# Optimization experiments

Measured on AMD Instinct MI355X. Metric: run time of the kernel, lower is better.

The kernel has to match this reference:

```python
import jax, jax.numpy as jnp
import numpy as np

APERTURE = 128
LN_EPS = 1e-6

def _layer_norm(y, g, b):
    mu = jnp.mean(y, axis=-1, keepdims=True)
    var = jnp.var(y, axis=-1, keepdims=True)
    return (y - mu) / jnp.sqrt(var + LN_EPS) * g + b

def setup_inputs() -> dict:
    key = jax.random.key(0)
    ks = jax.random.split(key, 12)
    B, S, D = 4, 4096, 1024
    gain = np.sqrt(2.0)
    xav = lambda k, fan_out, fan_in: jax.random.uniform(
        k, (fan_out, fan_in), jnp.float32,
        -gain * np.sqrt(6.0 / (fan_in + fan_out)), gain * np.sqrt(6.0 / (fan_in + fan_out)))
    return {
        "x": jax.random.normal(ks[0], (B, S, D), jnp.float32),
        "Wq": xav(ks[1], D, D),
        "Wk": xav(ks[2], D, D),
        "Wv": xav(ks[3], D, D),
        "Wo": xav(ks[4], D, D),
        "k1_w": xav(ks[5], D, D),
        "k1_b": jnp.full((D,), 0.1, jnp.float32),
        "k2_w": xav(ks[6], 1, D),
        "k2_b": jnp.full((1,), 0.1, jnp.float32),
        "ln_g": jnp.ones((D,), jnp.float32),
        "ln_b": jnp.zeros((D,), jnp.float32),
    }

def reference(x, Wq, Wk, Wv, Wo, k1_w, k1_b, k2_w, k2_b, ln_g, ln_b):
    B, S, D = x.shape
    scale = jnp.float32(1.0 / np.sqrt(D))
    neg_inf = jnp.float32(-np.inf)

    Q = x @ Wq.T  # [B,S,D]
    K = x @ Wk.T
    V = x @ Wv.T

    e = jnp.einsum('bsd,btd->bst', Q, K) * scale  # [B,S,S]

    # ignore_self: -inf on the diagonal
    i = jnp.arange(S)[:, None]
    j = jnp.arange(S)[None, :]
    e = jnp.where(i == j, neg_inf, e)

    # banded aperture mask: tril(e, ap) * triu(e, -ap); zeros of the product -> -inf
    d = j - i
    scope = jnp.where(d <= APERTURE, e, 0.0) * jnp.where(d >= -APERTURE, e, 0.0)
    e = jnp.where(scope == 0.0, neg_inf, e)

    alpha = jax.nn.softmax(e, axis=2)
    c = jnp.einsum('bst,btd->bsd', alpha, V)
    c = c @ Wo.T

    y = c + x
    y = _layer_norm(y, ln_g, ln_b)
    y = jax.nn.relu(y @ k1_w.T + k1_b)
    y = _layer_norm(y, ln_g, ln_b)
    y = jax.nn.sigmoid(y @ k2_w.T + k2_b)  # [B,S,1]
    return y.reshape(B, S)
```

## Files before the change

### kernel.cpp

```cpp
#include <hip/hip_runtime.h>
#include <math.h>

#define DD 1024
#define SS 4096
#define AP 128
#define LN_EPS 1e-6f
#define BK 32
#define BAND 384

typedef __bf16 bf16;
typedef __attribute__((ext_vector_type(4))) __bf16 bf16x4;
typedef __attribute__((ext_vector_type(8))) __bf16 bf16x8;
typedef __attribute__((ext_vector_type(4))) float f32x4;

#define GLOAD_LDS16(g, l)                                                   \
    __builtin_amdgcn_global_load_lds(                                        \
        (const __attribute__((address_space(1))) void*)(g),                  \
        (__attribute__((address_space(3))) void*)(l), 16, 0, 0)

__global__ __launch_bounds__(256) void cast_f2b(const float* __restrict__ s,
                                                bf16* __restrict__ d) {
    const int i = (blockIdx.x * 256 + threadIdx.x) * 4;
    const float4 a = *(const float4*)(s + i);
    bf16x4 o;
    o[0] = (__bf16)a.x; o[1] = (__bf16)a.y; o[2] = (__bf16)a.z; o[3] = (__bf16)a.w;
    *(bf16x4*)(d + i) = o;
}

__global__ __launch_bounds__(256) void prep_w(const float* __restrict__ Wo,
                                              const float* __restrict__ k1w,
                                              const float* __restrict__ lng,
                                              const float* __restrict__ Wq,
                                              const float* __restrict__ Wk,
                                              const float* __restrict__ Wv,
                                              bf16* __restrict__ Wob,
                                              bf16* __restrict__ k1g,
                                              bf16* __restrict__ Wtb) {
    const int z = blockIdx.y;
    if (z < 2) {
        const float* s = z ? k1w : Wo;
        bf16* d = z ? k1g : Wob;
        const int i = (blockIdx.x * 256 + threadIdx.x) * 4;
        float4 a = *(const float4*)(s + i);
        if (z) {
            const float4 g4 = *(const float4*)(lng + (i & (DD - 1)));
            a.x *= g4.x; a.y *= g4.y; a.z *= g4.z; a.w *= g4.w;
        }
        bf16x4 o;
        o[0] = (__bf16)a.x; o[1] = (__bf16)a.y; o[2] = (__bf16)a.z; o[3] = (__bf16)a.w;
        *(bf16x4*)(d + i) = o;
        return;
    }
    if (blockIdx.x >= 256) return;
    __shared__ float tile[64][65];
    const float* in = (z == 2) ? Wq : (z == 3) ? Wk : Wv;
    bf16* out = Wtb + ((size_t)(z - 2) << 20);
    const int r0 = (blockIdx.x >> 4) * 64, c0 = (blockIdx.x & 15) * 64;
    const int lr = threadIdx.x >> 4;
    const int lc = (threadIdx.x & 15) * 4;
#pragma unroll
    for (int rr = 0; rr < 4; rr++) {
        const int row = lr + rr * 16;
        const float4 v = *(const float4*)(in + (size_t)(r0 + row) * DD + c0 + lc);
        tile[row][lc] = v.x; tile[row][lc + 1] = v.y;
        tile[row][lc + 2] = v.z; tile[row][lc + 3] = v.w;
    }
    __syncthreads();
#pragma unroll
    for (int rr = 0; rr < 4; rr++) {
        const int row = lr + rr * 16;
        bf16x4 o;
        o[0] = (__bf16)tile[lc + 0][row];
        o[1] = (__bf16)tile[lc + 1][row];
        o[2] = (__bf16)tile[lc + 2][row];
        o[3] = (__bf16)tile[lc + 3][row];
        *(bf16x4*)(out + (size_t)(c0 + row) * DD + r0 + lc) = o;
    }
}

__global__ __launch_bounds__(256) void prep_vec(const float* __restrict__ k1w,
                                                const float* __restrict__ lng,
                                                const float* __restrict__ lnb,
                                                const float* __restrict__ k1b,
                                                float* __restrict__ u1,
                                                float* __restrict__ c1b) {
    const int lane = threadIdx.x & 63, wave = threadIdx.x >> 6;
    const int n = blockIdx.x * 4 + wave;
    const float* row = k1w + (size_t)n * DD + lane * 16;
    float su = 0.f, sb = 0.f;
#pragma unroll
    for (int q = 0; q < 4; q++) {
        const float4 a = *(const float4*)(row + q * 4);
        const float4 g4 = *(const float4*)(lng + lane * 16 + q * 4);
        const float4 b4 = *(const float4*)(lnb + lane * 16 + q * 4);
        su += a.x * g4.x + a.y * g4.y + a.z * g4.z + a.w * g4.w;
        sb += a.x * b4.x + a.y * b4.y + a.z * b4.z + a.w * b4.w;
    }
#pragma unroll
    for (int off = 32; off > 0; off >>= 1) {
        su += __shfl_xor(su, off);
        sb += __shfl_xor(sb, off);
    }
    if (lane == 0) {
        u1[n] = su;
        c1b[n] = sb + k1b[n];
    }
}

__global__ __launch_bounds__(256) void gemm_pair(const bf16* __restrict__ A0,
                                                 const bf16* __restrict__ W0,
                                                 bf16* __restrict__ O0,
                                                 const bf16* __restrict__ A1,
                                                 const bf16* __restrict__ W1,
                                                 bf16* __restrict__ O1) {
    const bf16* A = blockIdx.z ? A1 : A0;
    const bf16* W = blockIdx.z ? W1 : W0;
    bf16* O = blockIdx.z ? O1 : O0;
    __shared__ bf16 As[128 * BK];
    __shared__ bf16 Bs[128 * BK];
    const int tid = threadIdx.x;
    const int lane = tid & 63;
    const int wave = tid >> 6;
    const int wm = wave & 1;
    const int wn = wave >> 1;
    const int m0 = blockIdx.y * 128;
    const int n0 = blockIdx.x * 128;

    const int c = wave * 64 + lane;
    const int ar = c >> 2;
    const int ac = (c & 3) << 3;
    char* AsB = (char*)As;
    char* BsB = (char*)Bs;
    const int lr = lane & 15;
    const int lk = (lane >> 4) << 3;

    f32x4 acc[4][4] = {};

    for (int kt = 0; kt < DD; kt += BK) {
        const bf16* ga0 = A + (size_t)(m0 + ar) * DD + kt + ac;
        const bf16* gb0 = W + (size_t)(n0 + ar) * DD + kt + ac;
        GLOAD_LDS16(ga0, AsB + wave * 1024);
        GLOAD_LDS16(ga0 + (size_t)64 * DD, AsB + 4096 + wave * 1024);
        GLOAD_LDS16(gb0, BsB + wave * 1024);
        GLOAD_LDS16(gb0 + (size_t)64 * DD, BsB + 4096 + wave * 1024);
        __syncthreads();

        bf16x8 af[4], bfr[4];
#pragma unroll
        for (int i = 0; i < 4; i++)
            af[i] = *(const bf16x8*)&As[(wm * 64 + i * 16 + lr) * BK + lk];
#pragma unroll
        for (int j = 0; j < 4; j++)
            bfr[j] = *(const bf16x8*)&Bs[(wn * 64 + j * 16 + lr) * BK + lk];
#pragma unroll
        for (int i = 0; i < 4; i++)
#pragma unroll
            for (int j = 0; j < 4; j++)
                acc[i][j] = __builtin_amdgcn_mfma_f32_16x16x32_bf16(af[i], bfr[j], acc[i][j], 0, 0, 0);
        __syncthreads();
    }

#pragma unroll
    for (int i = 0; i < 4; i++) {
        const int row = m0 + wm * 64 + i * 16 + ((lane >> 4) << 2);
#pragma unroll
        for (int j = 0; j < 4; j++) {
            const int col = n0 + wn * 64 + j * 16 + (lane & 15);
#pragma unroll
            for (int rr = 0; rr < 4; rr++)
                O[(size_t)(row + rr) * DD + col] = (__bf16)acc[i][j][rr];
        }
    }
}

__global__ __launch_bounds__(512) void gemm_uv(const bf16* __restrict__ xb,
                                               const bf16* __restrict__ Gt,
                                               const bf16* __restrict__ W2,
                                               bf16* __restrict__ Ub,
                                               bf16* __restrict__ Vt2) {
    __shared__ bf16 As[256 * BK];
    __shared__ bf16 Bs[128 * BK];
    int id = blockIdx.x;
    const bf16* A;
    const bf16* W;
    bf16* O;
    int m0, n0, ldo;
    if (id < 512) {
        A = xb; W = Gt; O = Ub;
        m0 = (id & 63) * 256; n0 = (id >> 6) * 128; ldo = DD;
    } else {
        id -= 512;
        A = W2; W = xb; O = Vt2;
        m0 = (id >> 7) * 256; n0 = (id & 127) * 128; ldo = 4 * SS;
    }
    const int tid = threadIdx.x;
    const int lane = tid & 63;
    const int wave = tid >> 6;
    const int wm = wave & 3;
    const int wn = wave >> 2;

    const int ar = tid >> 2;
    const int ac = (tid & 3) << 3;
    char* AsB = (char*)As;
    char* BsB = (char*)Bs;
    const int lr = lane & 15;
    const int lk = (lane >> 4) << 3;

    f32x4 acc[4][4] = {};

    for (int kt = 0; kt < DD; kt += BK) {
        const bf16* ga0 = A + (size_t)(m0 + ar) * DD + kt + ac;
        const bf16* gb0 = W + (size_t)(n0 + ar) * DD + kt + ac;
        GLOAD_LDS16(ga0, AsB + wave * 1024);
        GLOAD_LDS16(ga0 + (size_t)128 * DD, AsB + 8192 + wave * 1024);
        GLOAD_LDS16(gb0, BsB + wave * 1024);
        __syncthreads();

        bf16x8 af[4], bfr[4];
#pragma unroll
        for (int i = 0; i < 4; i++)
            af[i] = *(const bf16x8*)&As[(wm * 64 + i * 16 + lr) * BK + lk];
#pragma unroll
        for (int j = 0; j < 4; j++)
            bfr[j] = *(const bf16x8*)&Bs[(wn * 64 + j * 16 + lr) * BK + lk];
#pragma unroll
        for (int i = 0; i < 4; i++)
#pragma unroll
            for (int j = 0; j < 4; j++)
                acc[i][j] = __builtin_amdgcn_mfma_f32_16x16x32_bf16(af[i], bfr[j], acc[i][j], 0, 0, 0);
        __syncthreads();
    }

#pragma unroll
    for (int i = 0; i < 4; i++) {
        const int row = m0 + wm * 64 + i * 16 + ((lane >> 4) << 2);
#pragma unroll
        for (int j = 0; j < 4; j++) {
            const int col = n0 + wn * 64 + j * 16 + (lane & 15);
#pragma unroll
            for (int rr = 0; rr < 4; rr++)
                O[(size_t)(row + rr) * ldo + col] = (__bf16)acc[i][j][rr];
        }
    }
}

__global__ __launch_bounds__(512) void gemm_k1(const bf16* __restrict__ T,
                                               const bf16* __restrict__ k1g,
                                               const float* __restrict__ mu,
                                               const float* __restrict__ rstd,
                                               const float* __restrict__ u1,
                                               const float* __restrict__ c1b,
                                               bf16* __restrict__ H0) {
    __shared__ bf16 As[256 * BK];
    __shared__ bf16 Bs[128 * BK];
    const int m0 = blockIdx.x * 256;
    const int n0 = blockIdx.y * 128;
    const int tid = threadIdx.x;
    const int lane = tid & 63;
    const int wave = tid >> 6;
    const int wm = wave & 3;
    const int wn = wave >> 2;

    const int ar = tid >> 2;
    const int ac = (tid & 3) << 3;
    char* AsB = (char*)As;
    char* BsB = (char*)Bs;
    const int lr = lane & 15;
    const int lk = (lane >> 4) << 3;

    f32x4 acc[4][4] = {};

    for (int kt = 0; kt < DD; kt += BK) {
        const bf16* ga0 = T + (size_t)(m0 + ar) * DD + kt + ac;
        const bf16* gb0 = k1g + (size_t)(n0 + ar) * DD + kt + ac;
        GLOAD_LDS16(ga0, AsB + wave * 1024);
        GLOAD_LDS16(ga0 + (size_t)128 * DD, AsB + 8192 + wave * 1024);
        GLOAD_LDS16(gb0, BsB + wave * 1024);
        __syncthreads();

        bf16x8 af[4], bfr[4];
#pragma unroll
        for (int i = 0; i < 4; i++)
            af[i] = *(const bf16x8*)&As[(wm * 64 + i * 16 + lr) * BK + lk];
#pragma unroll
        for (int j = 0; j < 4; j++)
            bfr[j] = *(const bf16x8*)&Bs[(wn * 64 + j * 16 + lr) * BK + lk];
#pragma unroll
        for (int i = 0; i < 4; i++)
#pragma unroll
            for (int j = 0; j < 4; j++)
                acc[i][j] = __builtin_amdgcn_mfma_f32_16x16x32_bf16(af[i], bfr[j], acc[i][j], 0, 0, 0);
        __syncthreads();
    }

#pragma unroll
    for (int i = 0; i < 4; i++) {
        const int row = m0 + wm * 64 + i * 16 + ((lane >> 4) << 2);
#pragma unroll
        for (int j = 0; j < 4; j++) {
            const int col = n0 + wn * 64 + j * 16 + (lane & 15);
            const float u1c = u1[col];
            const float cbc = c1b[col];
#pragma unroll
            for (int rr = 0; rr < 4; rr++) {
                const int r = row + rr;
                const float v = rstd[r] * (acc[i][j][rr] - mu[r] * u1c) + cbc;
                H0[(size_t)r * DD + col] = (__bf16)fmaxf(v, 0.f);
            }
        }
    }
}

__global__ __launch_bounds__(256) void attn_s_mfma(const bf16* __restrict__ U,
                                                   const bf16* __restrict__ X,
                                                   float* __restrict__ S) {
    __shared__ bf16 As[128 * BK];
    __shared__ bf16 Bs[128 * BK];
    const int tid = threadIdx.x;
    const int lane = tid & 63;
    const int wave = tid >> 6;
    const int wm = wave & 1;
    const int wn = wave >> 1;
    const int t = blockIdx.y;
    const int m0 = t * 128;
    const long w0 = (long)t * 128 - 128 + (long)blockIdx.x * 128;

    const int c = wave * 64 + lane;
    const int ar = c >> 2;
    const int ac = (c & 3) << 3;
    char* AsB = (char*)As;
    char* BsB = (char*)Bs;
    const int lr = lane & 15;
    const int lk = (lane >> 4) << 3;

    f32x4 acc[4][4] = {};

    for (int kt = 0; kt < DD; kt += BK) {
        const bf16* ga0 = U + (size_t)(m0 + ar) * DD + kt + ac;
        const bf16* gb0 = X + (w0 + ar) * DD + kt + ac;
        GLOAD_LDS16(ga0, AsB + wave * 1024);
        GLOAD_LDS16(ga0 + (size_t)64 * DD, AsB + 4096 + wave * 1024);
        GLOAD_LDS16(gb0, BsB + wave * 1024);
        GLOAD_LDS16(gb0 + (size_t)64 * DD, BsB + 4096 + wave * 1024);
        __syncthreads();

        bf16x8 af[4], bfr[4];
#pragma unroll
        for (int i = 0; i < 4; i++)
            af[i] = *(const bf16x8*)&As[(wm * 64 + i * 16 + lr) * BK + lk];
#pragma unroll
        for (int j = 0; j < 4; j++)
            bfr[j] = *(const bf16x8*)&Bs[(wn * 64 + j * 16 + lr) * BK + lk];
#pragma unroll
        for (int i = 0; i < 4; i++)
#pragma unroll
            for (int j = 0; j < 4; j++)
                acc[i][j] = __builtin_amdgcn_mfma_f32_16x16x32_bf16(af[i], bfr[j], acc[i][j], 0, 0, 0);
        __syncthreads();
    }

#pragma unroll
    for (int i = 0; i < 4; i++) {
        const int row = m0 + wm * 64 + i * 16 + ((lane >> 4) << 2);
#pragma unroll
        for (int j = 0; j < 4; j++) {
            const int col = blockIdx.x * 128 + wn * 64 + j * 16 + (lane & 15);
#pragma unroll
            for (int rr = 0; rr < 4; rr++)
                S[(size_t)(row + rr) * BAND + col] = acc[i][j][rr];
        }
    }
}

__global__ __launch_bounds__(256) void attn_softmax(const float* __restrict__ S,
                                                    bf16* __restrict__ P) {
    const int wave = threadIdx.x >> 6;
    const int lane = threadIdx.x & 63;
    const int g = blockIdx.x * 4 + wave;
    const int i = g & (SS - 1);
    const int j_start = ((i >> 7) << 7) - 128;
    const float scale = 0.03125f;
    float s[6];
    float m = -INFINITY;
#pragma unroll
    for (int t = 0; t < 6; t++) {
        const int jj = lane + t * 64;
        const int j = j_start + jj;
        const int dj = j - i;
        const bool valid = (j >= 0) && (j < SS) && (dj != 0) && (dj <= AP) && (dj >= -AP);
        const float v = S[(size_t)g * BAND + jj] * scale;
        s[t] = valid ? v : -INFINITY;
        m = fmaxf(m, s[t]);
    }
#pragma unroll
    for (int off = 32; off > 0; off >>= 1) m = fmaxf(m, __shfl_xor(m, off));
    float l = 0.f;
#pragma unroll
    for (int t = 0; t < 6; t++) {
        s[t] = __expf(s[t] - m);
        l += s[t];
    }
#pragma unroll
    for (int off = 32; off > 0; off >>= 1) l += __shfl_xor(l, off);
    const float inv = 1.f / l;
#pragma unroll
    for (int t = 0; t < 6; t++)
        P[(size_t)g * BAND + lane + t * 64] = (__bf16)(s[t] * inv);
}

__global__ __launch_bounds__(256) void attn_pv_mfma(const bf16* __restrict__ P,
                                                    const bf16* __restrict__ Vt,
                                                    const float* __restrict__ resid,
                                                    bf16* __restrict__ T) {
    __shared__ bf16 As[128 * BK];
    __shared__ bf16 Bs[128 * BK];
    const int tid = threadIdx.x;
    const int lane = tid & 63;
    const int wave = tid >> 6;
    const int wm = wave & 1;
    const int wn = wave >> 1;
    const int t = blockIdx.y;
    const int m0 = t * 128;
    const int n0 = blockIdx.x * 128;
    const bf16* Wb = Vt + (long)t * 128 - 128;

    const int c = wave * 64 + lane;
    const int ar = c >> 2;
    const int ac = (c & 3) << 3;
    char* AsB = (char*)As;
    char* BsB = (char*)Bs;
    const int lr = lane & 15;
    const int lk = (lane >> 4) << 3;

    f32x4 acc[4][4] = {};

    for (int kt = 0; kt < BAND; kt += BK) {
        const bf16* ga0 = P + (size_t)(m0 + ar) * BAND + kt + ac;
        const bf16* gb0 = Wb + (size_t)(n0 + ar) * (4 * SS) + kt + ac;
        GLOAD_LDS16(ga0, AsB + wave * 1024);
        GLOAD_LDS16(ga0 + (size_t)64 * BAND, AsB + 4096 + wave * 1024);
        GLOAD_LDS16(gb0, BsB + wave * 1024);
        GLOAD_LDS16(gb0 + (size_t)64 * (4 * SS), BsB + 4096 + wave * 1024);
        __syncthreads();

        bf16x8 af[4], bfr[4];
#pragma unroll
        for (int i = 0; i < 4; i++)
            af[i] = *(const bf16x8*)&As[(wm * 64 + i * 16 + lr) * BK + lk];
#pragma unroll
        for (int j = 0; j < 4; j++)
            bfr[j] = *(const bf16x8*)&Bs[(wn * 64 + j * 16 + lr) * BK + lk];
#pragma unroll
        for (int i = 0; i < 4; i++)
#pragma unroll
            for (int j = 0; j < 4; j++)
                acc[i][j] = __builtin_amdgcn_mfma_f32_16x16x32_bf16(af[i], bfr[j], acc[i][j], 0, 0, 0);
        __syncthreads();
    }

#pragma unroll
    for (int i = 0; i < 4; i++) {
        const int row = m0 + wm * 64 + i * 16 + ((lane >> 4) << 2);
#pragma unroll
        for (int j = 0; j < 4; j++) {
            const int col = n0 + wn * 64 + j * 16 + (lane & 15);
#pragma unroll
            for (int rr = 0; rr < 4; rr++) {
                const size_t idx = (size_t)(row + rr) * DD + col;
                T[idx] = (__bf16)(acc[i][j][rr] + resid[idx]);
            }
        }
    }
}

__global__ __launch_bounds__(256) void row_stats(const bf16* __restrict__ T,
                                                 float* __restrict__ mu,
                                                 float* __restrict__ rstd) {
    const int lane = threadIdx.x & 63, wave = threadIdx.x >> 6;
    const int r = blockIdx.x * 4 + wave;
    const bf16* h = T + (size_t)r * DD + lane * 16;
    const bf16x8 h0 = *(const bf16x8*)(h);
    const bf16x8 h1 = *(const bf16x8*)(h + 8);
    float s1 = 0.f, s2 = 0.f;
#pragma unroll
    for (int e = 0; e < 8; e++) {
        const float a = (float)h0[e];
        const float b = (float)h1[e];
        s1 += a + b;
        s2 += a * a + b * b;
    }
#pragma unroll
    for (int off = 32; off > 0; off >>= 1) {
        s1 += __shfl_xor(s1, off);
        s2 += __shfl_xor(s2, off);
    }
    if (lane == 0) {
        const float m = s1 * (1.f / DD);
        const float var = s2 * (1.f / DD) - m * m;
        mu[r] = m;
        rstd[r] = rsqrtf(var + LN_EPS);
    }
}

__global__ __launch_bounds__(256) void ln_k2_head(const bf16* __restrict__ H0,
                                                  const float* __restrict__ g,
                                                  const float* __restrict__ bta,
                                                  const float* __restrict__ w2,
                                                  const float* __restrict__ b2,
                                                  float* __restrict__ out) {
    __shared__ float ug[DD];
    __shared__ float red[256], red2[256];
    const int tid = threadIdx.x;
    const float4 g4 = *(const float4*)(g + tid * 4);
    const float4 w4 = *(const float4*)(w2 + tid * 4);
    const float4 b4 = *(const float4*)(bta + tid * 4);
    float4 u4;
    u4.x = g4.x * w4.x; u4.y = g4.y * w4.y; u4.z = g4.z * w4.z; u4.w = g4.w * w4.w;
    *(float4*)(ug + tid * 4) = u4;
    red[tid] = u4.x + u4.y + u4.z + u4.w;
    red2[tid] = b4.x * w4.x + b4.y * w4.y + b4.z * w4.z + b4.w * w4.w;
    __syncthreads();
    for (int s = 128; s > 0; s >>= 1) {
        if (tid < s) { red[tid] += red[tid + s]; red2[tid] += red2[tid + s]; }
        __syncthreads();
    }
    const float sum_u = red[0];
    const float sum_bw = red2[0];

    const int lane = tid & 63, wave = tid >> 6;
    const int r = blockIdx.x * 4 + wave;
    const bf16* h = H0 + (size_t)r * DD + lane * 16;
    const bf16x8 h0 = *(const bf16x8*)(h);
    const bf16x8 h1 = *(const bf16x8*)(h + 8);
    float s1 = 0.f, s2 = 0.f, s3 = 0.f;
#pragma unroll
    for (int e = 0; e < 8; e++) {
        const float a = (float)h0[e];
        const float b = (float)h1[e];
        const float ua = ug[lane * 16 + e];
        const float ub = ug[lane * 16 + 8 + e];
        s1 += a + b;
        s2 += a * a + b * b;
        s3 += a * ua + b * ub;
    }
#pragma unroll
    for (int off = 32; off > 0; off >>= 1) {
        s1 += __shfl_xor(s1, off);
        s2 += __shfl_xor(s2, off);
        s3 += __shfl_xor(s3, off);
    }
    if (lane == 0) {
        const float m = s1 * (1.f / DD);
        const float var = s2 * (1.f / DD) - m * m;
        const float rs = rsqrtf(var + LN_EPS);
        const float z = rs * (s3 - m * sum_u) + sum_bw + b2[0];
        out[r] = 1.f / (1.f + __expf(-z));
    }
}

extern "C" void kernel_launch(void* const* d_in, const int* in_sizes, int n_in,
                              void* d_out, int out_size, void* d_ws, size_t ws_size,
                              hipStream_t stream) {
    const float* x   = (const float*)d_in[0];
    const float* Wq  = (const float*)d_in[1];
    const float* Wk  = (const float*)d_in[2];
    const float* Wv  = (const float*)d_in[3];
    const float* Wo  = (const float*)d_in[4];
    const float* k1w = (const float*)d_in[5];
    const float* k1b = (const float*)d_in[6];
    const float* k2w = (const float*)d_in[7];
    const float* k2b = (const float*)d_in[8];
    const float* lng = (const float*)d_in[9];
    const float* lnb = (const float*)d_in[10];
    float* out = (float*)d_out;

    const int N = 4 * SS;
    char* ws = (char*)d_ws;
    bf16*  Ub   = (bf16*)(ws);
    bf16*  xb   = (bf16*)(ws + ((size_t)32  << 20));
    bf16*  Vt2  = (bf16*)(ws + ((size_t)64  << 20));
    bf16*  P    = (bf16*)(ws + ((size_t)96  << 20));
    float* S    = (float*)(ws + ((size_t)108 << 20));
    bf16*  H0   = (bf16*)(ws + ((size_t)132 << 20));
    bf16*  T    = (bf16*)(ws + ((size_t)164 << 20));
    bf16*  Wtb  = (bf16*)(ws + ((size_t)196 << 20));
    bf16*  Wqtb = Wtb;
    bf16*  Wktb = Wqtb + (1 << 20);
    bf16*  Wvtb = Wktb + (1 << 20);
    bf16*  Wob  = Wvtb + (1 << 20);
    bf16*  k1g  = Wob  + (1 << 20);
    bf16*  Gtb  = k1g  + (1 << 20);
    bf16*  W2b  = Gtb  + (1 << 20);
    float* muv  = (float*)(ws + ((size_t)210 << 20));
    float* rsd  = muv + N;
    float* u1   = rsd + N;
    float* c1b  = u1 + DD;

    dim3 tb(256);

    cast_f2b<<<N * DD / 1024, tb, 0, stream>>>(x, xb);
    prep_w<<<dim3(1024, 5), tb, 0, stream>>>(Wo, k1w, lng, Wq, Wk, Wv, Wob, k1g, Wtb);
    prep_vec<<<DD / 4, tb, 0, stream>>>(k1w, lng, lnb, k1b, u1, c1b);

    gemm_pair<<<dim3(8, 8, 2), tb, 0, stream>>>(Wktb, Wqtb, Gtb, Wob, Wvtb, W2b);

    gemm_uv<<<1024, dim3(512), 0, stream>>>(xb, Gtb, W2b, Ub, Vt2);

    attn_s_mfma<<<dim3(3, N / 128), tb, 0, stream>>>(Ub, xb, S);
    attn_softmax<<<N / 4, tb, 0, stream>>>(S, P);
    attn_pv_mfma<<<dim3(8, N / 128), tb, 0, stream>>>(P, Vt2, x, T);

    row_stats<<<N / 4, tb, 0, stream>>>(T, muv, rsd);
    gemm_k1<<<dim3(64, 8), dim3(512), 0, stream>>>(T, k1g, muv, rsd, u1, c1b, H0);
    ln_k2_head<<<N / 4, tb, 0, stream>>>(H0, lng, lnb, k2w, k2b, out);
}
```

Baseline: 375.7 us.

## Fuse LayerNorm statistics into GEMM epilogues and merge prep kernels

The three weight/input prep kernels are merged into one launch. The attention PV kernel now emits per-strip partial row sums and sums of squares, so row_stats only reduces small partials instead of rereading T. The k1 GEMM epilogue now computes partial LN and head-dot sums directly rather than writing H0. This removes the 32MB H0 write and its reread, plus the T reread. The residual now comes from bf16 x instead of fp32 x, which slightly changes precision.

```diff
diff --git a/kernel.cpp b/kernel.cpp
--- a/kernel.cpp
+++ b/kernel.cpp
@@ -18,31 +18,41 @@
         (const __attribute__((address_space(1))) void*)(g),                  \
         (__attribute__((address_space(3))) void*)(l), 16, 0, 0)
 
-__global__ __launch_bounds__(256) void cast_f2b(const float* __restrict__ s,
-                                                bf16* __restrict__ d) {
-    const int i = (blockIdx.x * 256 + threadIdx.x) * 4;
-    const float4 a = *(const float4*)(s + i);
-    bf16x4 o;
-    o[0] = (__bf16)a.x; o[1] = (__bf16)a.y; o[2] = (__bf16)a.z; o[3] = (__bf16)a.w;
-    *(bf16x4*)(d + i) = o;
-}
-
-__global__ __launch_bounds__(256) void prep_w(const float* __restrict__ Wo,
-                                              const float* __restrict__ k1w,
-                                              const float* __restrict__ lng,
-                                              const float* __restrict__ Wq,
-                                              const float* __restrict__ Wk,
-                                              const float* __restrict__ Wv,
-                                              bf16* __restrict__ Wob,
-                                              bf16* __restrict__ k1g,
-                                              bf16* __restrict__ Wtb) {
-    const int z = blockIdx.y;
-    if (z < 2) {
-        const float* s = z ? k1w : Wo;
-        bf16* d = z ? k1g : Wob;
-        const int i = (blockIdx.x * 256 + threadIdx.x) * 4;
+__global__ __launch_bounds__(256) void prep_all(const float* __restrict__ x,
+                                                const float* __restrict__ Wq,
+                                                const float* __restrict__ Wk,
+                                                const float* __restrict__ Wv,
+                                                const float* __restrict__ Wo,
+                                                const float* __restrict__ k1w,
+                                                const float* __restrict__ k1b,
+                                                const float* __restrict__ lng,
+                                                const float* __restrict__ lnb,
+                                                bf16* __restrict__ xb,
+                                                bf16* __restrict__ Wob,
+                                                bf16* __restrict__ k1g,
+                                                bf16* __restrict__ Wtb,
+                                                float* __restrict__ u1,
+                                                float* __restrict__ c1b) {
+    __shared__ float tile[64][65];
+    const int bid = blockIdx.x;
+    const int tid = threadIdx.x;
+    if (bid < 16384) {
+        const int i = (bid * 256 + tid) * 4;
+        const float4 a = *(const float4*)(x + i);
+        bf16x4 o;
+        o[0] = (__bf16)a.x; o[1] = (__bf16)a.y; o[2] = (__bf16)a.z; o[3] = (__bf16)a.w;
+        *(bf16x4*)(xb + i) = o;
+        return;
+    }
+    if (bid < 18432) {
+        const int b2 = bid - 16384;
+        const int sel = b2 >> 10;
+        const int bb = b2 & 1023;
+        const float* s = sel ? k1w : Wo;
+        bf16* d = sel ? k1g : Wob;
+        const int i = (bb * 256 + tid) * 4;
         float4 a = *(const float4*)(s + i);
-        if (z) {
+        if (sel) {
             const float4 g4 = *(const float4*)(lng + (i & (DD - 1)));
             a.x *= g4.x; a.y *= g4.y; a.z *= g4.z; a.w *= g4.w;
         }
@@ -51,41 +61,38 @@
         *(bf16x4*)(d + i) = o;
         return;
     }
-    if (blockIdx.x >= 256) return;
-    __shared__ float tile[64][65];
-    const float* in = (z == 2) ? Wq : (z == 3) ? Wk : Wv;
-    bf16* out = Wtb + ((size_t)(z - 2) << 20);
-    const int r0 = (blockIdx.x >> 4) * 64, c0 = (blockIdx.x & 15) * 64;
-    const int lr = threadIdx.x >> 4;
-    const int lc = (threadIdx.x & 15) * 4;
-#pragma unroll
-    for (int rr = 0; rr < 4; rr++) {
-        const int row = lr + rr * 16;
-        const float4 v = *(const float4*)(in + (size_t)(r0 + row) * DD + c0 + lc);
-        tile[row][lc] = v.x; tile[row][lc + 1] = v.y;
-        tile[row][lc + 2] = v.z; tile[row][lc + 3] = v.w;
-    }
-    __syncthreads();
-#pragma unroll
-    for (int rr = 0; rr < 4; rr++) {
-        const int row = lr + rr * 16;
-        bf16x4 o;
-        o[0] = (__bf16)tile[lc + 0][row];
-        o[1] = (__bf16)tile[lc + 1][row];
-        o[2] = (__bf16)tile[lc + 2][row];
-        o[3] = (__bf16)tile[lc + 3][row];
-        *(bf16x4*)(out + (size_t)(c0 + row) * DD + r0 + lc) = o;
-    }
-}
-
-__global__ __launch_bounds__(256) void prep_vec(const float* __restrict__ k1w,
-                                                const float* __restrict__ lng,
-                                                const float* __restrict__ lnb,
-                                                const float* __restrict__ k1b,
-                                                float* __restrict__ u1,
-                                                float* __restrict__ c1b) {
-    const int lane = threadIdx.x & 63, wave = threadIdx.x >> 6;
-    const int n = blockIdx.x * 4 + wave;
+    if (bid < 19200) {
+        const int t = bid - 18432;
+        const int tz = t >> 8;
+        const int tb_ = t & 255;
+        const float* in = (tz == 0) ? Wq : (tz == 1) ? Wk : Wv;
+        bf16* out = Wtb + ((size_t)tz << 20);
+        const int r0 = (tb_ >> 4) * 64, c0 = (tb_ & 15) * 64;
+        const int lr = tid >> 4;
+        const int lc = (tid & 15) * 4;
+#pragma unroll
+        for (int rr = 0; rr < 4; rr++) {
+            const int row = lr + rr * 16;
+            const float4 v = *(const float4*)(in + (size_t)(r0 + row) * DD + c0 + lc);
+            tile[row][lc] = v.x; tile[row][lc + 1] = v.y;
+            tile[row][lc + 2] = v.z; tile[row][lc + 3] = v.w;
+        }
+        __syncthreads();
+#pragma unroll
+        for (int rr = 0; rr < 4; rr++) {
+            const int row = lr + rr * 16;
+            bf16x4 o;
+            o[0] = (__bf16)tile[lc + 0][row];
+            o[1] = (__bf16)tile[lc + 1][row];
+            o[2] = (__bf16)tile[lc + 2][row];
+            o[3] = (__bf16)tile[lc + 3][row];
+            *(bf16x4*)(out + (size_t)(c0 + row) * DD + r0 + lc) = o;
+        }
+        return;
+    }
+    const int pv = bid - 19200;
+    const int lane = tid & 63, wave = tid >> 6;
+    const int n = pv * 4 + wave;
     const float* row = k1w + (size_t)n * DD + lane * 16;
     float su = 0.f, sb = 0.f;
 #pragma unroll
@@ -250,7 +257,9 @@
                                                const float* __restrict__ rstd,
                                                const float* __restrict__ u1,
                                                const float* __restrict__ c1b,
-                                               bf16* __restrict__ H0) {
+                                               const float* __restrict__ lng,
+                                               const float* __restrict__ k2w,
+                                               float* __restrict__ part_h) {
     __shared__ bf16 As[256 * BK];
     __shared__ bf16 Bs[128 * BK];
     const int m0 = blockIdx.x * 256;
@@ -293,19 +302,37 @@
         __syncthreads();
     }
 
+    float u1v[4], cbv[4], ugv[4];
+#pragma unroll
+    for (int j = 0; j < 4; j++) {
+        const int col = n0 + wn * 64 + j * 16 + (lane & 15);
+        u1v[j] = u1[col];
+        cbv[j] = c1b[col];
+        ugv[j] = lng[col] * k2w[col];
+    }
+    const int strip = blockIdx.y * 2 + wn;
 #pragma unroll
     for (int i = 0; i < 4; i++) {
-        const int row = m0 + wm * 64 + i * 16 + ((lane >> 4) << 2);
-#pragma unroll
-        for (int j = 0; j < 4; j++) {
-            const int col = n0 + wn * 64 + j * 16 + (lane & 15);
-            const float u1c = u1[col];
-            const float cbc = c1b[col];
-#pragma unroll
-            for (int rr = 0; rr < 4; rr++) {
-                const int r = row + rr;
-                const float v = rstd[r] * (acc[i][j][rr] - mu[r] * u1c) + cbc;
-                H0[(size_t)r * DD + col] = (__bf16)fmaxf(v, 0.f);
+#pragma unroll
+        for (int rr = 0; rr < 4; rr++) {
+            const int row = m0 + wm * 64 + i * 16 + ((lane >> 4) << 2) + rr;
+            const float mr = mu[row], rs = rstd[row];
+            float s1 = 0.f, s2 = 0.f, s3 = 0.f;
+#pragma unroll
+            for (int j = 0; j < 4; j++) {
+                const float v = rs * (acc[i][j][rr] - mr * u1v[j]) + cbv[j];
+                const float h = fmaxf(v, 0.f);
+                s1 += h; s2 += h * h; s3 += h * ugv[j];
+            }
+#pragma unroll
+            for (int off = 8; off > 0; off >>= 1) {
+                s1 += __shfl_xor(s1, off);
+                s2 += __shfl_xor(s2, off);
+                s3 += __shfl_xor(s3, off);
+            }
+            if ((lane & 15) == 0) {
+                float* p = part_h + (size_t)row * 48 + strip * 3;
+                p[0] = s1; p[1] = s2; p[2] = s3;
             }
         }
     }
@@ -410,8 +437,9 @@
 
 __global__ __launch_bounds__(256) void attn_pv_mfma(const bf16* __restrict__ P,
                                                     const bf16* __restrict__ Vt,
-                                                    const float* __restrict__ resid,
-                                                    bf16* __restrict__ T) {
+                                                    const bf16* __restrict__ xres,
+                                                    bf16* __restrict__ T,
+                                                    float* __restrict__ part_t) {
     __shared__ bf16 As[128 * BK];
     __shared__ bf16 Bs[128 * BK];
     const int tid = threadIdx.x;
@@ -458,66 +486,65 @@
         __syncthreads();
     }
 
+    const int strip = blockIdx.x * 2 + wn;
 #pragma unroll
     for (int i = 0; i < 4; i++) {
-        const int row = m0 + wm * 64 + i * 16 + ((lane >> 4) << 2);
-#pragma unroll
-        for (int j = 0; j < 4; j++) {
-            const int col = n0 + wn * 64 + j * 16 + (lane & 15);
-#pragma unroll
-            for (int rr = 0; rr < 4; rr++) {
-                const size_t idx = (size_t)(row + rr) * DD + col;
-                T[idx] = (__bf16)(acc[i][j][rr] + resid[idx]);
+#pragma unroll
+        for (int rr = 0; rr < 4; rr++) {
+            const int row = m0 + wm * 64 + i * 16 + ((lane >> 4) << 2) + rr;
+            float s1 = 0.f, s2 = 0.f;
+#pragma unroll
+            for (int j = 0; j < 4; j++) {
+                const int col = n0 + wn * 64 + j * 16 + (lane & 15);
+                const size_t idx = (size_t)row * DD + col;
+                const __bf16 tv_b = (__bf16)(acc[i][j][rr] + (float)xres[idx]);
+                T[idx] = tv_b;
+                const float tv = (float)tv_b;
+                s1 += tv; s2 += tv * tv;
             }
-        }
-    }
-}
-
-__global__ __launch_bounds__(256) void row_stats(const bf16* __restrict__ T,
-                                                 float* __restrict__ mu,
-                                                 float* __restrict__ rstd) {
-    const int lane = threadIdx.x & 63, wave = threadIdx.x >> 6;
-    const int r = blockIdx.x * 4 + wave;
-    const bf16* h = T + (size_t)r * DD + lane * 16;
-    const bf16x8 h0 = *(const bf16x8*)(h);
-    const bf16x8 h1 = *(const bf16x8*)(h + 8);
+#pragma unroll
+            for (int off = 8; off > 0; off >>= 1) {
+                s1 += __shfl_xor(s1, off);
+                s2 += __shfl_xor(s2, off);
+            }
+            if ((lane & 15) == 0) {
+                float2 st; st.x = s1; st.y = s2;
+                *(float2*)(part_t + (size_t)row * 32 + strip * 2) = st;
+            }
+        }
+    }
+}
+
+__global__ __launch_bounds__(256) void row_stats_p(const float* __restrict__ part_t,
+                                                   float* __restrict__ mu,
+                                                   float* __restrict__ rstd) {
+    const int r = blockIdx.x * 256 + threadIdx.x;
+    const float* p = part_t + (size_t)r * 32;
     float s1 = 0.f, s2 = 0.f;
 #pragma unroll
-    for (int e = 0; e < 8; e++) {
-        const float a = (float)h0[e];
-        const float b = (float)h1[e];
-        s1 += a + b;
-        s2 += a * a + b * b;
-    }
-#pragma unroll
-    for (int off = 32; off > 0; off >>= 1) {
-        s1 += __shfl_xor(s1, off);
-        s2 += __shfl_xor(s2, off);
-    }
-    if (lane == 0) {
-        const float m = s1 * (1.f / DD);
-        const float var = s2 * (1.f / DD) - m * m;
-        mu[r] = m;
-        rstd[r] = rsqrtf(var + LN_EPS);
-    }
-}
-
-__global__ __launch_bounds__(256) void ln_k2_head(const bf16* __restrict__ H0,
-                                                  const float* __restrict__ g,
-                                                  const float* __restrict__ bta,
-                                                  const float* __restrict__ w2,
-                                                  const float* __restrict__ b2,
-                                                  float* __restrict__ out) {
-    __shared__ float ug[DD];
+    for (int s = 0; s < 8; s++) {
+        const float4 v = *(const float4*)(p + s * 4);
+        s1 += v.x + v.z;
+        s2 += v.y + v.w;
+    }
+    const float m = s1 * (1.f / DD);
+    const float var = s2 * (1.f / DD) - m * m;
+    mu[r] = m;
+    rstd[r] = rsqrtf(var + LN_EPS);
+}
+
+__global__ __launch_bounds__(256) void ln_k2_p(const float* __restrict__ part_h,
+                                               const float* __restrict__ g,
+                                               const float* __restrict__ bta,
+                                               const float* __restrict__ w2,
+                                               const float* __restrict__ b2,
+                                               float* __restrict__ out) {
     __shared__ float red[256], red2[256];
     const int tid = threadIdx.x;
     const float4 g4 = *(const float4*)(g + tid * 4);
     const float4 w4 = *(const float4*)(w2 + tid * 4);
     const float4 b4 = *(const float4*)(bta + tid * 4);
-    float4 u4;
-    u4.x = g4.x * w4.x; u4.y = g4.y * w4.y; u4.z = g4.z * w4.z; u4.w = g4.w * w4.w;
-    *(float4*)(ug + tid * 4) = u4;
-    red[tid] = u4.x + u4.y + u4.z + u4.w;
+    red[tid] = g4.x * w4.x + g4.y * w4.y + g4.z * w4.z + g4.w * w4.w;
     red2[tid] = b4.x * w4.x + b4.y * w4.y + b4.z * w4.z + b4.w * w4.w;
     __syncthreads();
     for (int s = 128; s > 0; s >>= 1) {
@@ -527,35 +554,20 @@
     const float sum_u = red[0];
     const float sum_bw = red2[0];
 
-    const int lane = tid & 63, wave = tid >> 6;
-    const int r = blockIdx.x * 4 + wave;
-    const bf16* h = H0 + (size_t)r * DD + lane * 16;
-    const bf16x8 h0 = *(const bf16x8*)(h);
-    const bf16x8 h1 = *(const bf16x8*)(h + 8);
+    const int r = blockIdx.x * 256 + tid;
+    const float* p = part_h + (size_t)r * 48;
     float s1 = 0.f, s2 = 0.f, s3 = 0.f;
 #pragma unroll
-    for (int e = 0; e < 8; e++) {
-        const float a = (float)h0[e];
-        const float b = (float)h1[e];
-        const float ua = ug[lane * 16 + e];
-        const float ub = ug[lane * 16 + 8 + e];
-        s1 += a + b;
-        s2 += a * a + b * b;
-        s3 += a * ua + b * ub;
-    }
-#pragma unroll
-    for (int off = 32; off > 0; off >>= 1) {
-        s1 += __shfl_xor(s1, off);
-        s2 += __shfl_xor(s2, off);
-        s3 += __shfl_xor(s3, off);
-    }
-    if (lane == 0) {
-        const float m = s1 * (1.f / DD);
-        const float var = s2 * (1.f / DD) - m * m;
-        const float rs = rsqrtf(var + LN_EPS);
-        const float z = rs * (s3 - m * sum_u) + sum_bw + b2[0];
-        out[r] = 1.f / (1.f + __expf(-z));
-    }
+    for (int s = 0; s < 16; s++) {
+        s1 += p[s * 3 + 0];
+        s2 += p[s * 3 + 1];
+        s3 += p[s * 3 + 2];
+    }
+    const float m = s1 * (1.f / DD);
+    const float var = s2 * (1.f / DD) - m * m;
+    const float rs = rsqrtf(var + LN_EPS);
+    const float z = rs * (s3 - m * sum_u) + sum_bw + b2[0];
+    out[r] = 1.f / (1.f + __expf(-z));
 }
 
 extern "C" void kernel_launch(void* const* d_in, const int* in_sizes, int n_in,
@@ -581,7 +593,6 @@
     bf16*  Vt2  = (bf16*)(ws + ((size_t)64  << 20));
     bf16*  P    = (bf16*)(ws + ((size_t)96  << 20));
     float* S    = (float*)(ws + ((size_t)108 << 20));
-    bf16*  H0   = (bf16*)(ws + ((size_t)132 << 20));
     bf16*  T    = (bf16*)(ws + ((size_t)164 << 20));
     bf16*  Wtb  = (bf16*)(ws + ((size_t)196 << 20));
     bf16*  Wqtb = Wtb;
@@ -591,16 +602,17 @@
     bf16*  k1g  = Wob  + (1 << 20);
     bf16*  Gtb  = k1g  + (1 << 20);
     bf16*  W2b  = Gtb  + (1 << 20);
-    float* muv  = (float*)(ws + ((size_t)210 << 20));
-    float* rsd  = muv + N;
-    float* u1   = rsd + N;
-    float* c1b  = u1 + DD;
+    float* muv    = (float*)(ws + ((size_t)210 << 20));
+    float* rsd    = muv + N;
+    float* u1     = rsd + N;
+    float* c1b    = u1 + DD;
+    float* part_t = (float*)(ws + ((size_t)211 << 20));
+    float* part_h = (float*)(ws + ((size_t)214 << 20));
 
     dim3 tb(256);
 
-    cast_f2b<<<N * DD / 1024, tb, 0, stream>>>(x, xb);
-    prep_w<<<dim3(1024, 5), tb, 0, stream>>>(Wo, k1w, lng, Wq, Wk, Wv, Wob, k1g, Wtb);
-    prep_vec<<<DD / 4, tb, 0, stream>>>(k1w, lng, lnb, k1b, u1, c1b);
+    prep_all<<<19456, tb, 0, stream>>>(x, Wq, Wk, Wv, Wo, k1w, k1b, lng, lnb,
+                                       xb, Wob, k1g, Wtb, u1, c1b);
 
     gemm_pair<<<dim3(8, 8, 2), tb, 0, stream>>>(Wktb, Wqtb, Gtb, Wob, Wvtb, W2b);
 
@@ -608,9 +620,9 @@
 
     attn_s_mfma<<<dim3(3, N / 128), tb, 0, stream>>>(Ub, xb, S);
     attn_softmax<<<N / 4, tb, 0, stream>>>(S, P);
-    attn_pv_mfma<<<dim3(8, N / 128), tb, 0, stream>>>(P, Vt2, x, T);
-
-    row_stats<<<N / 4, tb, 0, stream>>>(T, muv, rsd);
-    gemm_k1<<<dim3(64, 8), dim3(512), 0, stream>>>(T, k1g, muv, rsd, u1, c1b, H0);
-    ln_k2_head<<<N / 4, tb, 0, stream>>>(H0, lng, lnb, k2w, k2b, out);
-}
+    attn_pv_mfma<<<dim3(8, N / 128), tb, 0, stream>>>(P, Vt2, xb, T, part_t);
+
+    row_stats_p<<<N / 256, tb, 0, stream>>>(part_t, muv, rsd);
+    gemm_k1<<<dim3(64, 8), dim3(512), 0, stream>>>(T, k1g, muv, rsd, u1, c1b, lng, k2w, part_h);
+    ln_k2_p<<<N / 256, tb, 0, stream>>>(part_h, lng, lnb, k2w, k2b, out);
+}
```

Result: no change. 369.4 us (-1.7%).
